# Kernel optimization log

Hardware: AMD Instinct MI355X
Metric: run time of the kernel (lower is better)

## Reference

```python
import jax, jax.numpy as jnp
import numpy as np

N, C, K, B, G = 32768, 128, 16, 4, 8
SCALE, BASE = 2.0, 10000.0

def _bn(x, gamma, beta, eps=1e-5):
    # torch BatchNorm1d (training): stats over all axes except channel (last)
    axes = tuple(range(x.ndim - 1))
    mean = x.mean(axes)
    var = x.var(axes)
    return (x - mean) / jnp.sqrt(var + eps) * gamma + beta

def _cayley_rope(x, coord, S_param):
    c = x.shape[-1]
    S = jnp.triu(S_param, 1)
    S = S - S.T
    I = jnp.eye(c, dtype=x.dtype)
    P = jnp.linalg.solve(I + S, I - S)  # (I+S)^-1 (I-S)
    xr = x @ P.T
    dpa = c // 3 // 2 * 2          # dim per axis (even)
    dr = dpa * 3                   # rotated dims
    inv_freq = 1.0 / (BASE ** (jnp.arange(0, dpa, 2, dtype=jnp.float32) / dpa))
    cs = coord * SCALE
    def rot(f, c1):
        ang = c1[:, None] * inv_freq[None, :]
        s, co = jnp.sin(ang), jnp.cos(ang)
        fr, fi = jnp.split(f, 2, axis=-1)
        return jnp.concatenate([fr * co - fi * s, fr * s + fi * co], -1)
    parts = [rot(xr[:, i * dpa:(i + 1) * dpa], cs[:, i]) for i in range(3)]
    out = jnp.concatenate(parts + [xr[:, dr:]], -1)
    return out @ P

def setup_inputs() -> dict:
    key = jax.random.key(0)
    ks = jax.random.split(key, 24)
    w = lambda k, i, o, s=0.02: jax.random.normal(k, (i, o), jnp.float32) * s
    inp = {
        'feat': jax.random.normal(ks[0], (N, C), jnp.float32),
        'coord': jax.random.uniform(ks[1], (N, 3), jnp.float32) * 10.0,
        'reference_index': jax.random.randint(ks[2], (N, K), 0, N),
        'offset': jnp.arange(1, B + 1, dtype=jnp.int32) * (N // B),
        'Wq': w(ks[3], C, C), 'bq': jnp.zeros((C,)),
        'gq': jnp.ones((C,)), 'bnq': jnp.zeros((C,)),
        'Wk': w(ks[4], C, C), 'bk': jnp.zeros((C,)),
        'gk': jnp.ones((C,)), 'bnk': jnp.zeros((C,)),
        'Wv': w(ks[5], C, C), 'bv': jnp.zeros((C,)),
        'S_param': jax.random.normal(ks[6], (C, C), jnp.float32) * 0.01,
        'Ww1': w(ks[7], C, G), 'bw1': jnp.zeros((G,)),
        'gw': jnp.ones((G,)), 'bnw': jnp.zeros((G,)),
        'Ww2': w(ks[8], G, G), 'bw2': jnp.zeros((G,)),
        'Wg1': w(ks[9], 2 * C, C), 'bg1': jnp.zeros((C,)),
        'gg': jnp.ones((C,)), 'bng': jnp.zeros((C,)),
        'Wg2': w(ks[10], C, G, 0.001), 'bg2': jnp.full((G,), 3.0),
    }
    return inp

def reference(feat, coord, reference_index, offset, Wq, bq, gq, bnq, Wk, bk, gk, bnk,
              Wv, bv, S_param, Ww1, bw1, gw, bnw, Ww2, bw2, Wg1, bg1, gg, bng, Wg2, bg2):
    q_raw = jax.nn.relu(_bn(feat @ Wq + bq, gq, bnq))
    k_raw = jax.nn.relu(_bn(feat @ Wk + bk, gk, bnk))
    value = feat @ Wv + bv
    q = _cayley_rope(q_raw, coord, S_param)
    k = _cayley_rope(k_raw, coord, S_param)
    kg = k[reference_index]            # [N,K,C] gather
    vg = value[reference_index]        # [N,K,C]
    rel = kg - q[:, None, :]
    geom = jax.nn.relu(_bn(rel @ Ww1 + bw1, gw, bnw)) @ Ww2 + bw2  # [N,K,G]
    seg = jnp.searchsorted(offset, jnp.arange(N), side='right')
    gmax = jax.ops.segment_max(q_raw, seg, num_segments=B)
    gate_in = jnp.concatenate([q_raw, gmax[seg]], -1)              # [N,2C]
    gate = jax.nn.sigmoid(jax.nn.relu(_bn(gate_in @ Wg1 + bg1, gg, bng)) @ Wg2 + bg2)  # [N,G]
    refined = geom * (1.0 + gate[:, None, :])
    attn = jax.nn.softmax(refined, axis=1)
    mask = jnp.sign(reference_index + 1).astype(attn.dtype)
    attn = attn * mask[:, :, None]
    vg4 = vg.reshape(N, K, G, C // G)
    out = jnp.einsum('nkgi,nkg->ngi', vg4, attn).reshape(N, C)
    return out
```

## Files before the change

### kernel.cpp

```cpp
#include <hip/hip_runtime.h>
#include <math.h>

#define N_PTS 32768
#define C_DIM 128
#define K_NB  16
#define G_DIM 8

#define OF_PW     0
#define OF_STATQ  1024
#define OF_STATK  1280
#define OF_STATG1 1536
#define OF_STATH  1792
#define OF_UMAXP  1808
#define OF_UMAXN  2320
#define OF_GSG    2832
#define OF_WQT    4096
#define OF_WKT    12288
#define OF_WVT    20480
#define OF_WG1T   28672
#define OF_PTMIT  36864
#define OF_QW     65536
#define OF_KW     327680
#define OF_GATE   589824
#define OF_G1     1048576
#define OF_V      5242880

typedef short bf16x8 __attribute__((ext_vector_type(8)));
typedef float f32x4  __attribute__((ext_vector_type(4)));

#define LSTR 136

__device__ __forceinline__ unsigned f2bf(float f) {
  unsigned u = __float_as_uint(f);
  return (u + 0x7fffu + ((u >> 16) & 1u)) >> 16;
}
__device__ __forceinline__ float bf2f(short s) {
  return __uint_as_float(((unsigned)(unsigned short)s) << 16);
}
__device__ __forceinline__ unsigned fenc(float f) {
  unsigned b = __float_as_uint(f);
  return (b & 0x80000000u) ? ~b : (b | 0x80000000u);
}
__device__ __forceinline__ float fdec(unsigned u) {
  unsigned b = (u & 0x80000000u) ? (u & 0x7fffffffu) : ~u;
  return __uint_as_float(b);
}
__device__ __forceinline__ bf16x8 pack_bf8(float4 a, float4 b) {
  bf16x8 r;
  r[0] = (short)f2bf(a.x); r[1] = (short)f2bf(a.y);
  r[2] = (short)f2bf(a.z); r[3] = (short)f2bf(a.w);
  r[4] = (short)f2bf(b.x); r[5] = (short)f2bf(b.y);
  r[6] = (short)f2bf(b.z); r[7] = (short)f2bf(b.w);
  return r;
}

__device__ __forceinline__ void g2l16(const void* g, void* l) {
  __builtin_amdgcn_global_load_lds(
      (const __attribute__((address_space(1))) void*)g,
      (__attribute__((address_space(3))) void*)l, 16, 0, 0);
}

__device__ __forceinline__ void stage_async(short* dst, const short* __restrict__ src, int tid) {
  int lane = tid & 63, wv = tid >> 6;
  #pragma unroll
  for (int it = 0; it < 8; ++it) {
    int chunk = it*256 + wv*64;
    int D = (chunk + lane)*16;
    int gs = D ^ (((D >> 8) & 7) << 4);
    g2l16((const char*)src + gs, (char*)dst + chunk*16);
  }
}

__device__ __forceinline__ f32x4 mfma1(const short* Bb, const bf16x8* a4, int row, int quad) {
  f32x4 ac = {0.f, 0.f, 0.f, 0.f};
  int sx = (row & 7) << 4;
  #pragma unroll
  for (int ks = 0; ks < 4; ++ks) {
    const char* p = (const char*)Bb + (((row*256) + ks*64 + quad*16) ^ sx);
    ac = __builtin_amdgcn_mfma_f32_16x16x32_bf16(a4[ks], *(const bf16x8*)p, ac, 0, 0, 0);
  }
  return ac;
}

__global__ __launch_bounds__(256) void cayley(const float* __restrict__ Sp,
    const float* __restrict__ Ww1,
    const float* __restrict__ Wq, const float* __restrict__ Wk,
    const float* __restrict__ Wv, const float* __restrict__ Wg1,
    short* __restrict__ WqT, short* __restrict__ WkT,
    short* __restrict__ WvT, short* __restrict__ Wg1T,
    short* __restrict__ PTmIT, float* __restrict__ PW,
    float* __restrict__ statz)
{
  __shared__ __align__(16) short Ssh[128*LSTR];
  __shared__ float x0[128], x1[128];
  int bx = blockIdx.x, tid = threadIdx.x;
  if (bx >= 64) {
    if (bx < 80) {
      int idx = bx - 64, widx = idx >> 2, qr = idx & 3;
      const float* src = (widx == 0) ? Wq : (widx == 1) ? Wk : (widx == 2) ? Wv : Wg1;
      short* dst = (widx == 0) ? WqT : (widx == 1) ? WkT : (widx == 2) ? WvT : Wg1T;
      const float4* s4 = (const float4*)src;
      short* T = Ssh;
      #pragma unroll
      for (int it = 0; it < 4; ++it) {
        int q = it*256 + tid; int kloc = q >> 5, n4 = q & 31;
        float4 v = s4[(qr*32 + kloc)*32 + n4];
        T[(n4*4+0)*40 + kloc] = (short)f2bf(v.x);
        T[(n4*4+1)*40 + kloc] = (short)f2bf(v.y);
        T[(n4*4+2)*40 + kloc] = (short)f2bf(v.z);
        T[(n4*4+3)*40 + kloc] = (short)f2bf(v.w);
      }
      __syncthreads();
      #pragma unroll
      for (int it = 0; it < 2; ++it) {
        int i2 = it*256 + tid;
        int n = i2 >> 2, part = i2 & 3;
        uint4 val = *(const uint4*)&T[n*40 + part*8];
        *(uint4*)&dst[n*128 + qr*32 + part*8] = val;
      }
    } else {
      #pragma unroll
      for (int it = 0; it < 8; ++it) {
        int idx = it*256 + tid;
        if (idx < 1808) statz[idx] = 0.f;
      }
    }
    return;
  }
  int c0 = bx*2, c1 = c0 + 1;
  {
    const float4* s4 = (const float4*)Sp;
    #pragma unroll
    for (int it = 0; it < 16; ++it) {
      int idx = it*256 + tid;
      int i = idx >> 5, j0 = (idx & 31) * 4;
      float4 v = s4[idx];
      #pragma unroll
      for (int u = 0; u < 4; ++u) {
        int j = j0 + u;
        float val = (&v.x)[u];
        if (j > i) {
          unsigned b = f2bf(val);
          Ssh[i*LSTR + j] = (short)b;
          Ssh[j*LSTR + i] = (short)(b ^ 0x8000u);
        } else if (j == i) {
          Ssh[i*LSTR + j] = 0;
        }
      }
    }
  }
  if (tid < 128) {
    x0[tid] = (tid == c0) ? 1.f : 0.f;
    x1[tid] = (tid == c1) ? 1.f : 0.f;
  }
  __syncthreads();
  int i = tid >> 1, h = tid & 1;
  const short* srow = &Ssh[i*LSTR + h*64];
  for (int t = 0; t < 16; ++t) {
    float a0 = 0.f, a1 = 0.f;
    #pragma unroll
    for (int jq = 0; jq < 16; ++jq) {
      short4 sv = *(const short4*)&srow[jq*4];
      #pragma unroll
      for (int u = 0; u < 4; ++u) {
        float s = bf2f((&sv.x)[u]);
        int j = h*64 + jq*4 + u;
        a0 = fmaf(s, x0[j], a0);
        a1 = fmaf(s, x1[j], a1);
      }
    }
    a0 += __shfl_xor(a0, 1);
    a1 += __shfl_xor(a1, 1);
    __syncthreads();
    if (h == 0) {
      x0[i] = a0 + ((i == c0) ? 1.f : 0.f);
      x1[i] = a1 + ((i == c1) ? 1.f : 0.f);
    }
    __syncthreads();
  }
  if (tid < 128) {
    PTmIT[c0*128 + tid] = (short)f2bf(2.f*x0[tid] - ((tid == c0) ? 2.f : 0.f));
  } else {
    int t = tid - 128;
    PTmIT[c1*128 + t] = (short)f2bf(2.f*x1[t] - ((t == c1) ? 2.f : 0.f));
  }
  if (tid < 16) {
    int cc = tid >> 3, g = tid & 7;
    const float* xv = cc ? x1 : x0;
    int c = cc ? c1 : c0;
    float acc = 0.f;
    #pragma unroll 8
    for (int j = 0; j < 128; ++j) acc = fmaf(xv[j], Ww1[j*8 + g], acc);
    PW[c*8 + g] = 2.f*acc - Ww1[c*8 + g];
  }
}

__global__ __launch_bounds__(256, 2) void qkv_mfma(const float* __restrict__ feat,
    const short* __restrict__ WqT, const short* __restrict__ WkT, const short* __restrict__ WvT,
    const float* __restrict__ bq, const float* __restrict__ bk, const float* __restrict__ bv,
    short* __restrict__ Vb,
    float* __restrict__ statq, float* __restrict__ statk,
    unsigned* __restrict__ umaxp, unsigned* __restrict__ umaxn)
{
  __shared__ __align__(16) short Bb0[128*128];
  __shared__ __align__(16) short Bb1[128*128];
  __shared__ float ssum[2][128], ssq[2][128];
  __shared__ unsigned ump[128], umn[128];
  int tid = threadIdx.x, row0 = blockIdx.x * 64, seg = row0 >> 13;
  int lane = tid & 63, w = tid >> 6, l15 = lane & 15, quad = lane >> 4;
  stage_async(Bb0, WqT, tid);
  if (tid < 128) {
    ssum[0][tid] = 0.f; ssum[1][tid] = 0.f;
    ssq[0][tid] = 0.f;  ssq[1][tid] = 0.f;
    ump[tid] = 0u; umn[tid] = 0u;
  }
  bf16x8 af[4];
  {
    long rbase = (long)(row0 + w*16 + l15) * 128;
    #pragma unroll
    for (int ks = 0; ks < 4; ++ks) {
      int c0 = ks*32 + quad*8;
      float4 v0 = *(const float4*)&feat[rbase + c0];
      float4 v1 = *(const float4*)&feat[rbase + c0 + 4];
      af[ks] = pack_bf8(v0, v1);
    }
  }
  __syncthreads();
  stage_async(Bb1, WkT, tid);
  {
    #pragma unroll
    for (int nt = 0; nt < 8; ++nt) {
      f32x4 ac = mfma1(Bb0, af, nt*16 + l15, quad);
      int col = nt*16 + l15;
      float bb = bq[col];
      float s = 0.f, s2 = 0.f, mx = -1e30f, mn = 1e30f;
      #pragma unroll
      for (int r = 0; r < 4; ++r) {
        float raw = ac[r];
        float v = raw + bb;
        s += v; s2 = fmaf(v, v, s2);
        mx = fmaxf(mx, raw); mn = fminf(mn, raw);
      }
      s += __shfl_xor(s, 16); s += __shfl_xor(s, 32);
      s2 += __shfl_xor(s2, 16); s2 += __shfl_xor(s2, 32);
      mx = fmaxf(mx, __shfl_xor(mx, 16)); mx = fmaxf(mx, __shfl_xor(mx, 32));
      mn = fminf(mn, __shfl_xor(mn, 16)); mn = fminf(mn, __shfl_xor(mn, 32));
      if (lane < 16) {
        atomicAdd(&ssum[0][col], s); atomicAdd(&ssq[0][col], s2);
        atomicMax(&ump[col], fenc(mx)); atomicMax(&umn[col], fenc(-mn));
      }
    }
  }
  __syncthreads();
  stage_async(Bb0, WvT, tid);
  {
    #pragma unroll
    for (int nt = 0; nt < 8; ++nt) {
      f32x4 ac = mfma1(Bb1, af, nt*16 + l15, quad);
      int col = nt*16 + l15;
      float bb = bk[col];
      float s = 0.f, s2 = 0.f;
      #pragma unroll
      for (int r = 0; r < 4; ++r) {
        float v = ac[r] + bb;
        s += v; s2 = fmaf(v, v, s2);
      }
      s += __shfl_xor(s, 16); s += __shfl_xor(s, 32);
      s2 += __shfl_xor(s2, 16); s2 += __shfl_xor(s2, 32);
      if (lane < 16) { atomicAdd(&ssum[1][col], s); atomicAdd(&ssq[1][col], s2); }
    }
  }
  __syncthreads();
  {
    #pragma unroll
    for (int nt = 0; nt < 8; ++nt) {
      f32x4 ac = mfma1(Bb0, af, nt*16 + l15, quad);
      int col = nt*16 + l15;
      float bb = bv[col];
      #pragma unroll
      for (int r = 0; r < 4; ++r)
        Vb[(long)(row0 + w*16 + quad*4 + r)*128 + col] = (short)f2bf(ac[r] + bb);
    }
  }
  __syncthreads();
  if (tid < 128) {
    atomicAdd(&statq[tid], ssum[0][tid]); atomicAdd(&statq[128 + tid], ssq[0][tid]);
    atomicAdd(&statk[tid], ssum[1][tid]); atomicAdd(&statk[128 + tid], ssq[1][tid]);
    atomicMax(&umaxp[seg*128 + tid], ump[tid]);
    atomicMax(&umaxn[seg*128 + tid], umn[tid]);
  }
}

__global__ __launch_bounds__(128) void gprep(
    const float* __restrict__ statq,
    const float* __restrict__ gq, const float* __restrict__ bnq,
    const float* __restrict__ bq,
    const unsigned* __restrict__ umaxp, const unsigned* __restrict__ umaxn,
    const float* __restrict__ Wg1, const float* __restrict__ bg1,
    float* __restrict__ gsgO)
{
  __shared__ float gml[128];
  int s = blockIdx.x, tid = threadIdx.x;
  const float invn = 1.f / 32768.f;
  {
    float m = statq[tid]*invn, vv = fmaf(-m, m, statq[128 + tid]*invn);
    float a = rsqrtf(vv + 1e-5f) * gq[tid];
    float b = fmaf(-m, a, bnq[tid]);
    float cb2 = fmaf(a, bq[tid], b);
    float mx = fdec(umaxp[s*128 + tid]);
    float mn = -fdec(umaxn[s*128 + tid]);
    gml[tid] = fmaxf(0.f, fmaxf(fmaf(a, mx, cb2), fmaf(a, mn, cb2)));
  }
  __syncthreads();
  float acc = bg1[tid];
  #pragma unroll 8
  for (int j = 0; j < 128; ++j)
    acc = fmaf(gml[j], Wg1[(128 + j)*128 + tid], acc);
  gsgO[s*128 + tid] = acc;
}

__global__ __launch_bounds__(256, 2) void rqkw(
    const float* __restrict__ feat,
    const short* __restrict__ WqT, const short* __restrict__ WkT,
    const short* __restrict__ PTmIT, const short* __restrict__ Wg1T,
    const float* __restrict__ coord,
    const float* __restrict__ bq, const float* __restrict__ bk,
    const float* __restrict__ statq, const float* __restrict__ statk,
    const float* __restrict__ gq, const float* __restrict__ bnq,
    const float* __restrict__ gk, const float* __restrict__ bnk,
    const float* __restrict__ gsgG,
    const float* __restrict__ PW, const float* __restrict__ bw1,
    float* __restrict__ qw, float* __restrict__ kw,
    float* __restrict__ g1, float* __restrict__ statg1)
{
  __shared__ __align__(16) char arena[81920];
  short* Bb0  = (short*)arena;
  short* Bb1  = (short*)(arena + 32768);
  char*  bnS  = arena + 65536;
  float* xsq  = (float*)arena;
  float* xsk  = (float*)(arena + 33792);
  float* pws  = (float*)(arena + 67584);
  float* ssum4 = (float*)(arena + 71680);
  float* ssq4  = (float*)(arena + 73728);
  int tid = threadIdx.x, row0 = blockIdx.x * 64, seg = row0 >> 13;
  int lane = tid & 63, w = tid >> 6, l15 = lane & 15, quad = lane >> 4;
  stage_async(Bb0, WqT, tid);
  stage_async(Bb1, WkT, tid);
  bf16x8 af[4];
  {
    long rbase = (long)(row0 + w*16 + l15) * 128;
    #pragma unroll
    for (int ks = 0; ks < 4; ++ks) {
      int c0 = ks*32 + quad*8;
      float4 v0 = *(const float4*)&feat[rbase + c0];
      float4 v1 = *(const float4*)&feat[rbase + c0 + 4];
      af[ks] = pack_bf8(v0, v1);
    }
  }
  float caRq[8], cbRq[8], caRk[8], cbRk[8];
  {
    const float invn = 1.f / 32768.f;
    #pragma unroll
    for (int nt = 0; nt < 8; ++nt) {
      int col = nt*16 + l15;
      float m = statq[col]*invn, vv = fmaf(-m, m, statq[128 + col]*invn);
      float a = rsqrtf(vv + 1e-5f) * gq[col];
      float b = fmaf(-m, a, bnq[col]);
      caRq[nt] = a; cbRq[nt] = fmaf(a, bq[col], b);
      m = statk[col]*invn; vv = fmaf(-m, m, statk[128 + col]*invn);
      a = rsqrtf(vv + 1e-5f) * gk[col];
      b = fmaf(-m, a, bnk[col]);
      caRk[nt] = a; cbRk[nt] = fmaf(a, bk[col], b);
    }
  }
  float gsR[8];
  #pragma unroll
  for (int nt = 0; nt < 8; ++nt)
    gsR[nt] = gsgG[seg*128 + nt*16 + l15];
  __syncthreads();
  float bnl_q[32], bnl_k[32];
  {
    #pragma unroll
    for (int nt = 0; nt < 8; ++nt) {
      f32x4 ac = mfma1(Bb0, af, nt*16 + l15, quad);
      int col = nt*16 + l15;
      float A = caRq[nt], B = cbRq[nt];
      #pragma unroll
      for (int r = 0; r < 4; ++r) {
        float v = fmaxf(0.f, fmaf(A, ac[r], B));
        bnl_q[nt*4 + r] = v;
        int row = w*16 + quad*4 + r;
        int ba = (row*256 + col*2) ^ ((row & 7) << 4);
        *(short*)(bnS + ba) = (short)f2bf(v);
      }
    }
  }
  __syncthreads();
  stage_async(Bb0, PTmIT, tid);
  {
    #pragma unroll
    for (int nt = 0; nt < 8; ++nt) {
      f32x4 ac = mfma1(Bb1, af, nt*16 + l15, quad);
      float A = caRk[nt], B = cbRk[nt];
      #pragma unroll
      for (int r = 0; r < 4; ++r)
        bnl_k[nt*4 + r] = fmaxf(0.f, fmaf(A, ac[r], B));
    }
  }
  __syncthreads();
  stage_async(Bb1, Wg1T, tid);
  bf16x8 af2q[4];
  {
    int rowA = w*16 + l15, sx2 = (rowA & 7) << 4;
    #pragma unroll
    for (int ks = 0; ks < 4; ++ks)
      af2q[ks] = *(const bf16x8*)(bnS + ((rowA*256 + ks*64 + quad*16) ^ sx2));
  }
  f32x4 accv_q[8];
  #pragma unroll
  for (int nt = 0; nt < 8; ++nt)
    accv_q[nt] = mfma1(Bb0, af2q, nt*16 + l15, quad);
  __syncthreads();
  {
    #pragma unroll
    for (int nt = 0; nt < 8; ++nt) {
      int col = nt*16 + l15;
      #pragma unroll
      for (int r = 0; r < 4; ++r) {
        int row = w*16 + quad*4 + r;
        int ba = (row*256 + col*2) ^ ((row & 7) << 4);
        *(short*)(bnS + ba) = (short)f2bf(bnl_k[nt*4 + r]);
      }
    }
  }
  __syncthreads();
  bf16x8 af2k[4];
  {
    int rowA = w*16 + l15, sx2 = (rowA & 7) << 4;
    #pragma unroll
    for (int ks = 0; ks < 4; ++ks)
      af2k[ks] = *(const bf16x8*)(bnS + ((rowA*256 + ks*64 + quad*16) ^ sx2));
  }
  f32x4 accv_k[8];
  float sred[8], s2red[8];
  {
    #pragma unroll
    for (int nt = 0; nt < 8; ++nt) {
      accv_k[nt] = mfma1(Bb0, af2k, nt*16 + l15, quad);
      f32x4 ac = mfma1(Bb1, af2q, nt*16 + l15, quad);
      int col = nt*16 + l15;
      float gsv = gsR[nt];
      float s = 0.f, s2 = 0.f;
      #pragma unroll
      for (int r = 0; r < 4; ++r) {
        float v = ac[r] + gsv;
        g1[(long)(row0 + w*16 + quad*4 + r)*128 + col] = v;
        s += v; s2 = fmaf(v, v, s2);
      }
      s += __shfl_xor(s, 16); s += __shfl_xor(s, 32);
      s2 += __shfl_xor(s2, 16); s2 += __shfl_xor(s2, 32);
      sred[nt] = s; s2red[nt] = s2;
    }
  }
  __syncthreads();
  {
    #pragma unroll
    for (int nt = 0; nt < 8; ++nt) {
      int col = nt*16 + l15;
      #pragma unroll
      for (int r = 0; r < 4; ++r) {
        int row = w*16 + quad*4 + r;
        xsq[row*132 + col] = accv_q[nt][r] + bnl_q[nt*4 + r];
        xsk[row*132 + col] = accv_k[nt][r] + bnl_k[nt*4 + r];
      }
    }
  }
  #pragma unroll
  for (int it = 0; it < 4; ++it) { int idx = tid + it*256; pws[idx] = PW[idx]; }
  if (lane < 16) {
    #pragma unroll
    for (int nt = 0; nt < 8; ++nt) {
      ssum4[w*128 + nt*16 + l15] = sred[nt];
      ssq4[w*128 + nt*16 + l15] = s2red[nt];
    }
  }
  __syncthreads();
  if (tid < 128) {
    float s = (ssum4[tid] + ssum4[128 + tid]) + (ssum4[256 + tid] + ssum4[384 + tid]);
    float s2 = (ssq4[tid] + ssq4[128 + tid]) + (ssq4[256 + tid] + ssq4[384 + tid]);
    atomicAdd(&statg1[tid], s);
    atomicAdd(&statg1[128 + tid], s2);
  }
  #pragma unroll
  for (int it = 0; it < 16; ++it) {
    int idx = it*256 + tid;
    int r = idx >> 6, s = idx & 63;
    if (s < 63) {
      int a3 = s / 21, j = s - a3*21;
      int cr = a3*42 + j;
      float invf = exp2f((float)(2*j) * (-13.287712379549449f / 42.f));
      float ang = coord[(row0 + r)*3 + a3] * (2.0f * invf);
      float sn, co; sincosf(ang, &sn, &co);
      float fr = xsq[r*132 + cr], fi = xsq[r*132 + cr + 21];
      xsq[r*132 + cr]      = fr*co - fi*sn;
      xsq[r*132 + cr + 21] = fr*sn + fi*co;
      fr = xsk[r*132 + cr]; fi = xsk[r*132 + cr + 21];
      xsk[r*132 + cr]      = fr*co - fi*sn;
      xsk[r*132 + cr + 21] = fr*sn + fi*co;
    }
  }
  __syncthreads();
  #pragma unroll
  for (int it = 0; it < 4; ++it) {
    int idx = it*256 + tid;
    int mat = idx >> 9, r2 = (idx >> 3) & 63, g = idx & 7;
    const float* x2 = mat ? xsk : xsq;
    float a0 = 0.f, a1 = 0.f, a2 = 0.f, a3 = 0.f;
    #pragma unroll 8
    for (int i = 0; i < 128; i += 4) {
      float4 xv = *(const float4*)&x2[r2*132 + i];
      a0 = fmaf(xv.x, pws[(i+0)*8 + g], a0);
      a1 = fmaf(xv.y, pws[(i+1)*8 + g], a1);
      a2 = fmaf(xv.z, pws[(i+2)*8 + g], a2);
      a3 = fmaf(xv.w, pws[(i+3)*8 + g], a3);
    }
    float acc = (a0 + a1) + (a2 + a3) + (mat ? bw1[g] : 0.f);
    float* dst = mat ? kw : qw;
    dst[(long)(row0 + r2)*8 + g] = acc;
  }
}

__global__ __launch_bounds__(256) void hstat_k(
    const float* __restrict__ kw, const float* __restrict__ qw,
    const int* __restrict__ ref, float* __restrict__ stath)
{
  __shared__ float red[256];
  int tid = threadIdx.x;
  long base = (long)blockIdx.x * 4096;
  float s = 0.f, sq = 0.f;
  for (int it = 0; it < 16; ++it) {
    long idx = base + it*256 + tid;
    int n = (int)(idx >> 7); int kk = (int)((idx >> 3) & 15); int g = (int)(idx & 7);
    int r = ref[n*16 + kk];
    float h = kw[(long)r*8 + g] - qw[(long)n*8 + g];
    s += h; sq = fmaf(h, h, sq);
  }
  red[tid] = s; __syncthreads();
  for (int d = 128; d >= 8; d >>= 1) { if (tid < d) red[tid] += red[tid + d]; __syncthreads(); }
  if (tid < 8) atomicAdd(&stath[tid], red[tid]);
  __syncthreads();
  red[tid] = sq; __syncthreads();
  for (int d = 128; d >= 8; d >>= 1) { if (tid < d) red[tid] += red[tid + d]; __syncthreads(); }
  if (tid < 8) atomicAdd(&stath[8 + tid], red[tid]);
}

__global__ __launch_bounds__(256) void attn2(
    const float* __restrict__ g1, const float* __restrict__ statg1,
    const float* __restrict__ ggm, const float* __restrict__ bng,
    const float* __restrict__ Wg2, const float* __restrict__ bg2,
    const float* __restrict__ qw, const float* __restrict__ kw,
    const float* __restrict__ stath,
    const float* __restrict__ gw, const float* __restrict__ bnw,
    const float* __restrict__ Ww2, const float* __restrict__ bw2,
    const int* __restrict__ ref, const short* __restrict__ vb,
    float* __restrict__ out)
{
  __shared__ float gs[32][132];
  __shared__ float w2s[128][8];
  __shared__ float cA[128], cB[128];
  __shared__ float gt[32][8];
  __shared__ float sm1[2][16][9];
  __shared__ float sm2[2][16][9];
  __shared__ int   smr[2][16];
  int tid = threadIdx.x;
  int row0 = blockIdx.x * 32;
  #pragma unroll
  for (int it = 0; it < 4; ++it) { int idx = tid + it*256; w2s[idx >> 3][idx & 7] = Wg2[idx]; }
  if (tid < 128) {
    const float invn = 1.f / 32768.f;
    float m = statg1[tid]*invn, vv = fmaf(-m, m, statg1[128 + tid]*invn);
    float a = rsqrtf(vv + 1e-5f) * ggm[tid];
    cA[tid] = a; cB[tid] = fmaf(-m, a, bng[tid]);
  }
  #pragma unroll
  for (int it = 0; it < 4; ++it) {
    int idx = tid + it*256; int r = idx >> 5, cq = idx & 31;
    *(float4*)&gs[r][cq*4] = *(const float4*)&g1[(long)(row0 + r)*128 + cq*4];
  }
  __syncthreads();
  {
    int r = tid >> 3, g = tid & 7;
    float acc = bg2[g];
    #pragma unroll 8
    for (int c2 = 0; c2 < 128; ++c2) {
      float act = fmaxf(0.f, fmaf(gs[r][c2], cA[c2], cB[c2]));
      acc = fmaf(act, w2s[c2][g], acc);
    }
    gt[r][g] = 1.f / (1.f + expf(-acc));
  }
  int rh = tid >> 7, t = tid & 127;
  int kk = t >> 3, g = t & 7;
  const float invnk = 1.f / 524288.f;
  float m0 = stath[g]*invnk, v0 = fmaf(-m0, m0, stath[8 + g]*invnk);
  float aw = rsqrtf(v0 + 1e-5f) * gw[g];
  float bw = fmaf(-m0, aw, bnw[g]);
  float w2r[8];
  #pragma unroll
  for (int g2 = 0; g2 < 8; ++g2) w2r[g2] = Ww2[g2*8 + g];
  float bw2g = bw2[g];
  __syncthreads();
  for (int itr = 0; itr < 16; ++itr) {
    int nl = itr*2 + rh;
    int n = row0 + nl;
    if (t < 16) smr[rh][t] = ref[n*16 + t];
    __syncthreads();
    int rr = smr[rh][kk];
    float h = kw[(long)rr*8 + g] - qw[(long)n*8 + g];
    sm1[rh][kk][g] = fmaxf(0.f, fmaf(h, aw, bw));
    __syncthreads();
    float acc = bw2g;
    #pragma unroll
    for (int g2 = 0; g2 < 8; ++g2) acc = fmaf(sm1[rh][kk][g2], w2r[g2], acc);
    float refined = acc * (1.f + gt[nl][g]);
    sm2[rh][kk][g] = refined;
    __syncthreads();
    float mx = -1e30f;
    #pragma unroll
    for (int k2 = 0; k2 < 16; ++k2) mx = fmaxf(mx, sm2[rh][k2][g]);
    float e = expf(refined - mx);
    sm1[rh][kk][g] = e;
    __syncthreads();
    float ssum = 0.f;
    #pragma unroll
    for (int k2 = 0; k2 < 16; ++k2) ssum += sm1[rh][k2][g];
    float mask = ((rr + 1) > 0) ? 1.f : (((rr + 1) == 0) ? 0.f : -1.f);
    float attn = e / ssum * mask;
    sm2[rh][kk][g] = attn;
    __syncthreads();
    float o = 0.f;
    #pragma unroll
    for (int k2 = 0; k2 < 16; ++k2) {
      float vv = bf2f(vb[(long)smr[rh][k2]*128 + t]);
      o = fmaf(vv, sm2[rh][k2][t >> 4], o);
    }
    out[(long)n*128 + t] = o;
    __syncthreads();
  }
}

extern "C" void kernel_launch(void* const* d_in, const int* in_sizes, int n_in,
                              void* d_out, int out_size, void* d_ws, size_t ws_size,
                              hipStream_t stream)
{
  const float* feat  = (const float*)d_in[0];
  const float* coord = (const float*)d_in[1];
  const int*   ref   = (const int*)d_in[2];
  const float* Wq  = (const float*)d_in[4];
  const float* bq  = (const float*)d_in[5];
  const float* gq  = (const float*)d_in[6];
  const float* bnq = (const float*)d_in[7];
  const float* Wk  = (const float*)d_in[8];
  const float* bk  = (const float*)d_in[9];
  const float* gk  = (const float*)d_in[10];
  const float* bnk = (const float*)d_in[11];
  const float* Wv  = (const float*)d_in[12];
  const float* bv  = (const float*)d_in[13];
  const float* Sp  = (const float*)d_in[14];
  const float* Ww1 = (const float*)d_in[15];
  const float* bw1 = (const float*)d_in[16];
  const float* gw  = (const float*)d_in[17];
  const float* bnw = (const float*)d_in[18];
  const float* Ww2 = (const float*)d_in[19];
  const float* bw2 = (const float*)d_in[20];
  const float* Wg1 = (const float*)d_in[21];
  const float* bg1 = (const float*)d_in[22];
  const float* ggm = (const float*)d_in[23];
  const float* bng = (const float*)d_in[24];
  const float* Wg2 = (const float*)d_in[25];
  const float* bg2 = (const float*)d_in[26];
  float* out = (float*)d_out;

  float* W = (float*)d_ws;
  float* PW = W + OF_PW;
  short* WqT   = (short*)(W + OF_WQT);
  short* WkT   = (short*)(W + OF_WKT);
  short* WvT   = (short*)(W + OF_WVT);
  short* Wg1T  = (short*)(W + OF_WG1T);
  short* PTmIT = (short*)(W + OF_PTMIT);
  float* G1 = W + OF_G1;
  short* Vb = (short*)(W + OF_V);

  cayley<<<81, 256, 0, stream>>>(Sp, Ww1, Wq, Wk, Wv, Wg1,
                                 WqT, WkT, WvT, Wg1T, PTmIT, PW, W + OF_STATQ);
  qkv_mfma<<<512, 256, 0, stream>>>(feat, WqT, WkT, WvT, bq, bk, bv, Vb,
                                    W + OF_STATQ, W + OF_STATK,
                                    (unsigned*)(W + OF_UMAXP), (unsigned*)(W + OF_UMAXN));
  gprep<<<4, 128, 0, stream>>>(W + OF_STATQ, gq, bnq, bq,
                               (const unsigned*)(W + OF_UMAXP),
                               (const unsigned*)(W + OF_UMAXN),
                               Wg1, bg1, W + OF_GSG);
  rqkw<<<512, 256, 0, stream>>>(feat, WqT, WkT, PTmIT, Wg1T, coord,
                                bq, bk,
                                W + OF_STATQ, W + OF_STATK,
                                gq, bnq, gk, bnk,
                                W + OF_GSG, PW, bw1,
                                W + OF_QW, W + OF_KW, G1, W + OF_STATG1);
  hstat_k<<<1024, 256, 0, stream>>>(W + OF_KW, W + OF_QW, ref, W + OF_STATH);
  attn2<<<1024, 256, 0, stream>>>(G1, W + OF_STATG1, ggm, bng, Wg2, bg2,
                                  W + OF_QW, W + OF_KW, W + OF_STATH,
                                  gw, bnw, Ww2, bw2, ref, Vb, out);
}
```

Measured before the change: 289.4 us.

## Assign one wavefront per point in attn2, replacing block barriers with shuffles

```diff
diff --git a/kernel.cpp b/kernel.cpp
--- a/kernel.cpp
+++ b/kernel.cpp
@@ -569,9 +569,8 @@
   __shared__ float w2s[128][8];
   __shared__ float cA[128], cB[128];
   __shared__ float gt[32][8];
-  __shared__ float sm1[2][16][9];
-  __shared__ float sm2[2][16][9];
-  __shared__ int   smr[2][16];
+  __shared__ float ascr[4][128];
+  __shared__ int   rscr[4][16];
   int tid = threadIdx.x;
   int row0 = blockIdx.x * 32;
   #pragma unroll
@@ -598,53 +597,59 @@
     }
     gt[r][g] = 1.f / (1.f + expf(-acc));
   }
-  int rh = tid >> 7, t = tid & 127;
-  int kk = t >> 3, g = t & 7;
+  int w = tid >> 6, lane = tid & 63;
+  int gL = lane & 7;
+  int kL = lane >> 3;
   const float invnk = 1.f / 524288.f;
-  float m0 = stath[g]*invnk, v0 = fmaf(-m0, m0, stath[8 + g]*invnk);
-  float aw = rsqrtf(v0 + 1e-5f) * gw[g];
-  float bw = fmaf(-m0, aw, bnw[g]);
+  float m0 = stath[gL]*invnk, v0 = fmaf(-m0, m0, stath[8 + gL]*invnk);
+  float aw = rsqrtf(v0 + 1e-5f) * gw[gL];
+  float bw = fmaf(-m0, aw, bnw[gL]);
   float w2r[8];
   #pragma unroll
-  for (int g2 = 0; g2 < 8; ++g2) w2r[g2] = Ww2[g2*8 + g];
-  float bw2g = bw2[g];
-  __syncthreads();
-  for (int itr = 0; itr < 16; ++itr) {
-    int nl = itr*2 + rh;
+  for (int g2 = 0; g2 < 8; ++g2) w2r[g2] = Ww2[g2*8 + gL];
+  float bw2g = bw2[gL];
+  __syncthreads();
+  for (int it = 0; it < 8; ++it) {
+    int nl = it*4 + w;
     int n = row0 + nl;
-    if (t < 16) smr[rh][t] = ref[n*16 + t];
-    __syncthreads();
-    int rr = smr[rh][kk];
-    float h = kw[(long)rr*8 + g] - qw[(long)n*8 + g];
-    sm1[rh][kk][g] = fmaxf(0.f, fmaf(h, aw, bw));
-    __syncthreads();
-    float acc = bw2g;
-    #pragma unroll
-    for (int g2 = 0; g2 < 8; ++g2) acc = fmaf(sm1[rh][kk][g2], w2r[g2], acc);
-    float refined = acc * (1.f + gt[nl][g]);
-    sm2[rh][kk][g] = refined;
-    __syncthreads();
-    float mx = -1e30f;
-    #pragma unroll
-    for (int k2 = 0; k2 < 16; ++k2) mx = fmaxf(mx, sm2[rh][k2][g]);
-    float e = expf(refined - mx);
-    sm1[rh][kk][g] = e;
-    __syncthreads();
-    float ssum = 0.f;
-    #pragma unroll
-    for (int k2 = 0; k2 < 16; ++k2) ssum += sm1[rh][k2][g];
-    float mask = ((rr + 1) > 0) ? 1.f : (((rr + 1) == 0) ? 0.f : -1.f);
-    float attn = e / ssum * mask;
-    sm2[rh][kk][g] = attn;
-    __syncthreads();
-    float o = 0.f;
+    int rmy = 0;
+    if (lane < 16) { rmy = ref[n*16 + lane]; rscr[w][lane] = rmy; }
+    int rr0 = __shfl(rmy, kL);
+    int rr1 = __shfl(rmy, kL + 8);
+    float qv = qw[(long)n*8 + gL];
+    float s0 = fmaxf(0.f, fmaf(kw[(long)rr0*8 + gL] - qv, aw, bw));
+    float s1 = fmaxf(0.f, fmaf(kw[(long)rr1*8 + gL] - qv, aw, bw));
+    float a0 = bw2g, a1 = bw2g;
+    int gbase = kL*8;
+    #pragma unroll
+    for (int g2 = 0; g2 < 8; ++g2) {
+      a0 = fmaf(__shfl(s0, gbase + g2), w2r[g2], a0);
+      a1 = fmaf(__shfl(s1, gbase + g2), w2r[g2], a1);
+    }
+    float gtv1 = 1.f + gt[nl][gL];
+    float r0 = a0 * gtv1;
+    float r1 = a1 * gtv1;
+    float mx = fmaxf(r0, r1);
+    mx = fmaxf(mx, __shfl_xor(mx, 8));
+    mx = fmaxf(mx, __shfl_xor(mx, 16));
+    mx = fmaxf(mx, __shfl_xor(mx, 32));
+    float e0 = expf(r0 - mx), e1 = expf(r1 - mx);
+    float ss = e0 + e1;
+    ss += __shfl_xor(ss, 8); ss += __shfl_xor(ss, 16); ss += __shfl_xor(ss, 32);
+    float mask0 = ((rr0 + 1) > 0) ? 1.f : (((rr0 + 1) == 0) ? 0.f : -1.f);
+    float mask1 = ((rr1 + 1) > 0) ? 1.f : (((rr1 + 1) == 0) ? 0.f : -1.f);
+    ascr[w][lane]      = e0 / ss * mask0;
+    ascr[w][lane + 64] = e1 / ss * mask1;
+    float o0 = 0.f, o1 = 0.f;
     #pragma unroll
     for (int k2 = 0; k2 < 16; ++k2) {
-      float vv = bf2f(vb[(long)smr[rh][k2]*128 + t]);
-      o = fmaf(vv, sm2[rh][k2][t >> 4], o);
-    }
-    out[(long)n*128 + t] = o;
-    __syncthreads();
+      int rr = rscr[w][k2];
+      unsigned vv = *(const unsigned*)&vb[(long)rr*128 + 2*lane];
+      float a = ascr[w][k2*8 + kL];
+      o0 = fmaf(bf2f((short)(vv & 0xffffu)), a, o0);
+      o1 = fmaf(bf2f((short)(vv >> 16)), a, o1);
+    }
+    *(float2*)&out[(long)n*128 + 2*lane] = make_float2(o0, o1);
   }
 }
 
```

Measured after the change: 275.6 us. -4.8%, faster.
